# Optimization experiments

Measured on AMD Instinct MI355X. Metric: run time of the kernel, lower is better.

Reference implementation:

```python
import jax, jax.numpy as jnp
import numpy as np

N_INSTANCES = 32  # instance ids 1..32 assumed present (id 0 = background)


def setup_inputs() -> dict:
    key = jax.random.key(0)
    ks = jax.random.split(key, 6)
    B, F, H, W = 8, 64, 512, 512
    encoded = jax.random.normal(ks[0], (B, F, H, W), dtype=jnp.float32)
    masks = jax.random.randint(ks[1], (B, 1, H, W), 0, N_INSTANCES + 1, dtype=jnp.int32)
    w1 = jax.random.normal(ks[2], (2 * F, F // 2), dtype=jnp.float32) * (1.0 / np.sqrt(2 * F))
    b1 = jax.random.normal(ks[3], (F // 2,), dtype=jnp.float32) * 0.01
    w2 = jax.random.normal(ks[4], (F // 2, 4), dtype=jnp.float32) * (1.0 / np.sqrt(F // 2))
    b2 = jax.random.normal(ks[5], (4,), dtype=jnp.float32) * 0.01
    return {"encoded": encoded, "masks": masks, "w1": w1, "b1": b1, "w2": w2, "b2": b2}


def reference(encoded, masks, w1, b1, w2, b2):
    B, F, H, W = encoded.shape
    N = N_INSTANCES
    ids = masks[:, 0].reshape(B, H * W)                    # [B, HW] int ids 0..N
    feats = jnp.transpose(encoded, (0, 2, 3, 1)).reshape(B, H * W, F)  # [B, HW, F]
    # Original: cur_mask * encoded then max over H,W. Outside-mask pixels contribute 0,
    # so the result equals max(0, segment_max of features over the instance's pixels).
    seg = jax.vmap(lambda f, i: jax.ops.segment_max(f, i, num_segments=N + 1))(feats, ids)
    vectors = jnp.maximum(seg[:, 1:, :], 0.0)              # [B, N, F] (drop background id 0)
    # Pairwise relation MLP: pair(i, j) = concat(v_i, v_j)
    vi = jnp.broadcast_to(vectors[:, :, None, :], (B, N, N, F))
    vj = jnp.broadcast_to(vectors[:, None, :, :], (B, N, N, F))
    pair = jnp.concatenate([vi, vj], axis=-1)              # [B, N(i), N(j), 2F]
    h = jnp.einsum('bijk,kh->bijh', pair, w1) + b1         # [B, N, N, F//2]
    out = jax.nn.sigmoid(jnp.einsum('bijh,hc->bijc', h, w2) + b2)  # [B, N(i), N(j), C]
    # torch layout: connections[b, c, j, i]
    connections = jnp.transpose(out, (0, 3, 2, 1))         # [B, C, N, N]
    return vectors, connections
```

## Files before the change

### kernel.cpp

```cpp
#include <hip/hip_runtime.h>
#include <math.h>

#define HW    (512 * 512)
#define FCH   64
#define NB    8
#define NID   32
#define CHUNK 4096
#define ACC_STRIDE 33

__global__ __launch_bounds__(512) void segmax_kernel(
    const float* __restrict__ encoded,
    const int*   __restrict__ masks,
    float*       __restrict__ vectors)
{
    const int b      = blockIdx.y;
    const int chunk0 = blockIdx.x * CHUNK;
    const int tid    = threadIdx.x;
    const int wave   = tid >> 6;
    const int lane   = tid & 63;

    __shared__ int   ids[CHUNK];
    __shared__ float acc[FCH * ACC_STRIDE];

    for (int i = tid; i < FCH * ACC_STRIDE; i += 512)
        acc[i] = 0.0f;

    {
        const int4* msrc = (const int4*)(masks + (size_t)b * HW + chunk0);
        int4* mdst = (int4*)ids;
        for (int i = tid; i < CHUNK / 4; i += 512)
            mdst[i] = msrc[i];
    }
    __syncthreads();

    const float* ebase = encoded + (size_t)b * FCH * HW + chunk0;

    for (int k = 0; k < 8; ++k) {
        const int f = wave * 8 + k;
        const float4* src = (const float4*)(ebase + (size_t)f * HW);
        float* facc = acc + f * ACC_STRIDE;
#pragma unroll 4
        for (int it = 0; it < 16; ++it) {
            const int idx = it * 64 + lane;
            float4 v  = src[idx];
            int4   id = ((const int4*)ids)[idx];
            if (id.x > 0 && v.x > 0.0f) atomicMax((unsigned*)&facc[id.x - 1], __float_as_uint(v.x));
            if (id.y > 0 && v.y > 0.0f) atomicMax((unsigned*)&facc[id.y - 1], __float_as_uint(v.y));
            if (id.z > 0 && v.z > 0.0f) atomicMax((unsigned*)&facc[id.z - 1], __float_as_uint(v.z));
            if (id.w > 0 && v.w > 0.0f) atomicMax((unsigned*)&facc[id.w - 1], __float_as_uint(v.w));
        }
    }
    __syncthreads();

    for (int e = tid; e < FCH * NID; e += 512) {
        const int f = e >> 5;
        const int n = e & 31;
        const float m = acc[f * ACC_STRIDE + n];
        if (m > 0.0f)
            atomicMax((unsigned*)&vectors[((size_t)b * NID + n) * FCH + f],
                      __float_as_uint(m));
    }
}

__global__ __launch_bounds__(256) void conn_kernel(
    const float* __restrict__ vectors,
    const float* __restrict__ w1,
    const float* __restrict__ b1,
    const float* __restrict__ w2,
    const float* __restrict__ b2,
    float*       __restrict__ out)
{
    const int b   = blockIdx.x;
    const int tid = threadIdx.x;

    __shared__ float v[NID][FCH];
    __shared__ float A[FCH][4], Bm[FCH][4];
    __shared__ float s[NID][4], t[NID][4];
    __shared__ float cc[4];

    for (int i = tid; i < NID * FCH; i += 256)
        ((float*)v)[i] = vectors[(size_t)b * NID * FCH + i];

    {
        const int k = tid >> 2, c = tid & 3;
        float a = 0.0f, bb = 0.0f;
#pragma unroll
        for (int h = 0; h < 32; ++h) {
            const float w2v = w2[h * 4 + c];
            a  += w1[k * 32 + h]        * w2v;
            bb += w1[(k + 64) * 32 + h] * w2v;
        }
        A[k][c]  = a;
        Bm[k][c] = bb;
        if (tid < 4) {
            float x = b2[tid];
#pragma unroll
            for (int h = 0; h < 32; ++h) x += b1[h] * w2[h * 4 + tid];
            cc[tid] = x;
        }
    }
    __syncthreads();

    if (tid < 128) {
        const int i = tid >> 2, c = tid & 3;
        float a = 0.0f;
#pragma unroll
        for (int f = 0; f < FCH; ++f) a += v[i][f] * A[f][c];
        s[i][c] = a;
    } else {
        const int j = (tid - 128) >> 2, c = tid & 3;
        float a = 0.0f;
#pragma unroll
        for (int f = 0; f < FCH; ++f) a += v[j][f] * Bm[f][c];
        t[j][c] = a;
    }
    __syncthreads();

    for (int o = tid; o < 4 * NID * NID; o += 256) {
        const int i = o & 31;
        const int j = (o >> 5) & 31;
        const int c = o >> 10;
        const float x = s[i][c] + t[j][c] + cc[c];
        out[(((size_t)b * 4 + c) * NID + j) * NID + i] = 1.0f / (1.0f + expf(-x));
    }
}

extern "C" void kernel_launch(void* const* d_in, const int* in_sizes, int n_in,
                              void* d_out, int out_size, void* d_ws, size_t ws_size,
                              hipStream_t stream) {
    const float* encoded = (const float*)d_in[0];
    const int*   masks   = (const int*)d_in[1];
    const float* w1      = (const float*)d_in[2];
    const float* b1      = (const float*)d_in[3];
    const float* w2      = (const float*)d_in[4];
    const float* b2      = (const float*)d_in[5];
    float* out = (float*)d_out;

    float* vectors     = out;
    float* connections = out + NB * NID * FCH;

    hipMemsetAsync(vectors, 0, (size_t)NB * NID * FCH * sizeof(float), stream);

    segmax_kernel<<<dim3(HW / CHUNK, NB), 512, 0, stream>>>(encoded, masks, vectors);
    conn_kernel<<<NB, 256, 0, stream>>>(vectors, w1, b1, w2, b2, connections);
}
```

Measured before the change: 714.1 us.

## Privatize segment-max accumulators per wave with 8-way replicated LDS bins

```diff
diff --git a/kernel.cpp b/kernel.cpp
--- a/kernel.cpp
+++ b/kernel.cpp
@@ -5,8 +5,8 @@
 #define FCH   64
 #define NB    8
 #define NID   32
-#define CHUNK 4096
-#define ACC_STRIDE 33
+#define CHUNK 2048
+#define PRIV  (33 * 8)
 
 __global__ __launch_bounds__(512) void segmax_kernel(
     const float* __restrict__ encoded,
@@ -18,47 +18,46 @@
     const int tid    = threadIdx.x;
     const int wave   = tid >> 6;
     const int lane   = tid & 63;
+    const int g      = lane & 7;
 
     __shared__ int   ids[CHUNK];
-    __shared__ float acc[FCH * ACC_STRIDE];
+    __shared__ float priv[8 * PRIV];
 
-    for (int i = tid; i < FCH * ACC_STRIDE; i += 512)
-        acc[i] = 0.0f;
-
-    {
-        const int4* msrc = (const int4*)(masks + (size_t)b * HW + chunk0);
-        int4* mdst = (int4*)ids;
-        for (int i = tid; i < CHUNK / 4; i += 512)
-            mdst[i] = msrc[i];
-    }
+    ((int4*)ids)[tid] = ((const int4*)(masks + (size_t)b * HW + chunk0))[tid];
     __syncthreads();
 
+    float* pw = priv + wave * PRIV;
     const float* ebase = encoded + (size_t)b * FCH * HW + chunk0;
+    const float4 z4 = make_float4(0.0f, 0.0f, 0.0f, 0.0f);
 
     for (int k = 0; k < 8; ++k) {
         const int f = wave * 8 + k;
         const float4* src = (const float4*)(ebase + (size_t)f * HW);
-        float* facc = acc + f * ACC_STRIDE;
-#pragma unroll 4
-        for (int it = 0; it < 16; ++it) {
+
+        ((float4*)pw)[lane] = z4;
+        if (lane < 2) ((float4*)pw)[64 + lane] = z4;
+        asm volatile("s_waitcnt lgkmcnt(0)" ::: "memory");
+
+#pragma unroll
+        for (int it = 0; it < CHUNK / 256; ++it) {
             const int idx = it * 64 + lane;
-            float4 v  = src[idx];
-            int4   id = ((const int4*)ids)[idx];
-            if (id.x > 0 && v.x > 0.0f) atomicMax((unsigned*)&facc[id.x - 1], __float_as_uint(v.x));
-            if (id.y > 0 && v.y > 0.0f) atomicMax((unsigned*)&facc[id.y - 1], __float_as_uint(v.y));
-            if (id.z > 0 && v.z > 0.0f) atomicMax((unsigned*)&facc[id.z - 1], __float_as_uint(v.z));
-            if (id.w > 0 && v.w > 0.0f) atomicMax((unsigned*)&facc[id.w - 1], __float_as_uint(v.w));
+            const float4 v  = src[idx];
+            const int4   id = ((const int4*)ids)[idx];
+            atomicMax((unsigned*)&pw[(id.x << 3) + g], __float_as_uint(fmaxf(v.x, 0.0f)));
+            atomicMax((unsigned*)&pw[(id.y << 3) + g], __float_as_uint(fmaxf(v.y, 0.0f)));
+            atomicMax((unsigned*)&pw[(id.z << 3) + g], __float_as_uint(fmaxf(v.z, 0.0f)));
+            atomicMax((unsigned*)&pw[(id.w << 3) + g], __float_as_uint(fmaxf(v.w, 0.0f)));
         }
-    }
-    __syncthreads();
+        asm volatile("s_waitcnt lgkmcnt(0)" ::: "memory");
 
-    for (int e = tid; e < FCH * NID; e += 512) {
-        const int f = e >> 5;
-        const int n = e & 31;
-        const float m = acc[f * ACC_STRIDE + n];
-        if (m > 0.0f)
-            atomicMax((unsigned*)&vectors[((size_t)b * NID + n) * FCH + f],
+        const float4 m4 = ((const float4*)(pw + 8))[lane];
+        float m = fmaxf(fmaxf(m4.x, m4.y), fmaxf(m4.z, m4.w));
+        m = fmaxf(m, __shfl_xor(m, 1));
+        if ((lane & 1) == 0 && m > 0.0f) {
+            atomicMax((unsigned*)&vectors[((size_t)b * NID + (lane >> 1)) * FCH + f],
                       __float_as_uint(m));
+        }
+        asm volatile("s_waitcnt lgkmcnt(0)" ::: "memory");
     }
 }
 
```

Result: no change. 725.0 us (+1.5%).
